# Kernel tuning notes

Hardware: AMD Instinct MI355X
Metric: run time of the kernel (lower is better)

Reference implementation:

```python
import jax, jax.numpy as jnp
from jax import lax
import numpy as np

B, DIM, H, W = 1, 48, 192, 192
HEADS, K, DIL = 2, 7, 3
HD = DIM // HEADS
HID = int(DIM * 2.66)  # 127 (Restormer GEGLU hidden)
EPS = 1e-5


def _window_starts(L, Kk, D):
    # NATTEN window-start rule: keep phase i % D, shift window inside bounds.
    s = np.zeros(L, dtype=np.int32)
    for i in range(L):
        if D <= 1:
            st = max(i - Kk // 2, 0)
            if i + Kk // 2 >= L:
                st = L - Kk
        else:
            st = i - (Kk // 2) * D
            if st < 0:
                st = i % D
            elif i + (Kk // 2) * D >= L:
                imodd = i % D
                a = (L // D) * D
                b = L - a
                if imodd < b:
                    st = L - b + imodd - 2 * (Kk // 2) * D
                else:
                    st = a + imodd - Kk * D
        s[i] = st
    return s


def _nbr_tables(L, Kk, D):
    st = _window_starts(L, Kk, D)
    idx = st[:, None] + np.arange(Kk)[None, :] * D          # [L, K] absolute neighbor idx
    pb = (st - np.arange(L)) // D                            # signed offset of window start (in dilation units)
    pb = pb[:, None] + (Kk - 1) + np.arange(Kk)[None, :]     # [L, K] rpb index in [0, 2K-2]
    return jnp.asarray(idx), jnp.asarray(pb)

IH, PBH = _nbr_tables(H, K, DIL)
IW, PBW = _nbr_tables(W, K, DIL)


def layernorm(x, w, b):  # channel LN on NCHW (WithBias, biased var)
    mu = x.mean(1, keepdims=True)
    var = ((x - mu) ** 2).mean(1, keepdims=True)
    return (x - mu) / jnp.sqrt(var + EPS) * w[None, :, None, None] + b[None, :, None, None]


def na2d(x, qkv_w, qkv_b, rpb, proj_w, proj_b):
    # x: NCHW -> BHWC
    t = x.transpose(0, 2, 3, 1)
    qkv = t @ qkv_w.T + qkv_b                                # [B,H,W,3*DIM]
    qkv = qkv.reshape(B, H, W, 3, HEADS, HD)
    q, k, v = qkv[:, :, :, 0], qkv[:, :, :, 1], qkv[:, :, :, 2]
    q = q * (HD ** -0.5)
    # gather dilated 7x7 neighborhoods: [B, H, K, W, K, heads, hd]
    kn = k[:, IH[:, :, None, None], IW[None, None, :, :]]
    vn = v[:, IH[:, :, None, None], IW[None, None, :, :]]
    attn = jnp.einsum('bijnc,bixjync->bijnxy', q, kn)        # [B,H,W,heads,K,K]
    bias = rpb[:, PBH][:, :, :, PBW]                         # [heads,H,K,W,K]
    attn = attn + bias.transpose(1, 3, 0, 2, 4)
    attn = jax.nn.softmax(attn.reshape(B, H, W, HEADS, K * K), axis=-1)
    attn = attn.reshape(B, H, W, HEADS, K, K)
    out = jnp.einsum('bijnxy,bixjync->bijnc', attn, vn).reshape(B, H, W, DIM)
    out = out @ proj_w.T + proj_b
    return out.transpose(0, 3, 1, 2)


def chan_mod(x, eca_w):  # ECA-style gate: GAP -> 1D conv over channels -> sigmoid
    p = x.mean((2, 3))                                       # [B,C]
    y = lax.conv_general_dilated(p[:, None, :], eca_w[None, None, :], (1,), [(3, 3)],
                                 dimension_numbers=('NCH', 'OIH', 'NCH'))[:, 0, :]
    return jax.nn.sigmoid(y)[:, :, None, None]


def ffn(x, w_in, w_dw, w_out):  # conv-GEGLU
    t = jnp.einsum('bchw,oc->bohw', x, w_in)                 # 1x1: DIM -> 2*HID
    t = lax.conv_general_dilated(t, w_dw, (1, 1), [(1, 1), (1, 1)],
                                 feature_group_count=2 * HID,
                                 dimension_numbers=('NCHW', 'OIHW', 'NCHW'))
    x1, x2 = t[:, :HID], t[:, HID:]
    g = jax.nn.gelu(x1, approximate=False) * x2
    return jnp.einsum('bchw,oc->bohw', g, w_out)             # 1x1: HID -> DIM


def setup_inputs() -> dict:
    key = jax.random.key(0)
    ks = jax.random.split(key, 10)
    d = {
        'x': jax.random.normal(ks[0], (B, DIM, H, W), jnp.float32),
        'ln1_w': jnp.ones((DIM,), jnp.float32),
        'ln1_b': jnp.zeros((DIM,), jnp.float32),
        'qkv_w': jax.random.normal(ks[1], (3 * DIM, DIM), jnp.float32) * 0.05,
        'qkv_b': jnp.zeros((3 * DIM,), jnp.float32),
        'rpb': jax.random.normal(ks[2], (HEADS, 2 * K - 1, 2 * K - 1), jnp.float32) * 0.02,
        'proj_w': jax.random.normal(ks[3], (DIM, DIM), jnp.float32) * 0.05,
        'proj_b': jnp.zeros((DIM,), jnp.float32),
        'eca_w': jax.random.normal(ks[4], (7,), jnp.float32) * 0.1,
        'ln2_w': jnp.ones((DIM,), jnp.float32),
        'ln2_b': jnp.zeros((DIM,), jnp.float32),
        'w_in': jax.random.normal(ks[5], (2 * HID, DIM), jnp.float32) * 0.05,
        'w_dw': jax.random.normal(ks[6], (2 * HID, 1, 3, 3), jnp.float32) * 0.05,
        'w_out': jax.random.normal(ks[7], (DIM, HID), jnp.float32) * 0.05,
    }
    return d


def reference(x, ln1_w, ln1_b, qkv_w, qkv_b, rpb, proj_w, proj_b, eca_w,
              ln2_w, ln2_b, w_in, w_dw, w_out):
    xn1 = layernorm(x, ln1_w, ln1_b)
    x = x + na2d(xn1, qkv_w, qkv_b, rpb, proj_w, proj_b) * chan_mod(xn1, eca_w)
    x = x + ffn(layernorm(x, ln2_w, ln2_b), w_in, w_dw, w_out)
    return x
```

## Files before the change

### kernel.cpp

```cpp
#include <hip/hip_runtime.h>
#include <hip/hip_bf16.h>
#include <math.h>

#define HW_ (192*192)
#define Wd 192
#define HIDc 127
#define NBLK1 (HW_/64)

#define O_LN1W 0
#define O_QKVW 96
#define O_QKVB 7008
#define O_RPB  7152
#define O_PROJW 7490
#define O_PROJB 9794
#define O_ECA  9842
#define O_LN2W 9849
#define O_WIN  9945
#define O_WDW  22137
#define O_WOUT 24423
#define WTS_LEN 30519

typedef unsigned short ushort_t;

__device__ __forceinline__ float b2f(__hip_bfloat16 v){ return __bfloat162float(v); }
__device__ __forceinline__ float u2f(ushort_t h){ return __uint_as_float(((unsigned)h)<<16); }
__device__ __forceinline__ ushort_t f2u(float f){
    __hip_bfloat16 h = __float2bfloat16(f);
    union { __hip_bfloat16 b; ushort_t u; } c; c.b = h; return c.u;
}
__device__ __forceinline__ void up2(unsigned u, float& a, float& b){
    a = __uint_as_float(u << 16);
    b = __uint_as_float(u & 0xffff0000u);
}

__device__ __forceinline__ int wstart(int i){
    if (i < 9) return i % 3;
    if (i >= 183) return 171 + (i % 3);
    return i - 9;
}

__device__ __forceinline__ float dot48bf(const uint4* wr, const float* xr){
    float acc = 0.f;
    #pragma unroll
    for (int c8 = 0; c8 < 6; c8++){
        uint4 u = wr[c8];
        float f0,f1,f2,f3,f4,f5,f6,f7;
        up2(u.x,f0,f1); up2(u.y,f2,f3); up2(u.z,f4,f5); up2(u.w,f6,f7);
        acc += f0*xr[8*c8]   + f1*xr[8*c8+1] + f2*xr[8*c8+2] + f3*xr[8*c8+3]
             + f4*xr[8*c8+4] + f5*xr[8*c8+5] + f6*xr[8*c8+6] + f7*xr[8*c8+7];
    }
    return acc;
}

__global__ void convert_kernel(
    const void* p0, const void* p1, const void* p2, const void* p3,
    const void* p4, const void* p5, const void* p6, const void* p7,
    const void* p8, const void* p9, const void* p10, const void* p11,
    const void* p12, const ushort_t* __restrict__ xu, int* __restrict__ mode_out,
    float* __restrict__ wts, ushort_t* __restrict__ qkvbf, ushort_t* __restrict__ woutTbf,
    ushort_t* __restrict__ winbf, ushort_t* __restrict__ projbf)
{
    __shared__ int sbad;
    if (threadIdx.x == 0) sbad = 0;
    __syncthreads();
    {
        unsigned u = xu[2*threadIdx.x];
        float f = __uint_as_float(u << 16);
        if (!(fabsf(f) < 100.f)) atomicAdd(&sbad, 1);
    }
    __syncthreads();
    const int md = (sbad > 16) ? 1 : 0;
    if (blockIdx.x == 0 && threadIdx.x == 0) mode_out[0] = md;

    const void* ps[13] = {p0,p1,p2,p3,p4,p5,p6,p7,p8,p9,p10,p11,p12};
    const int sz[13]  = {48,48,6912,144,338,2304,48,7,48,48,12192,2286,6096};
    const int off[13] = {O_LN1W,48,O_QKVW,O_QKVB,O_RPB,O_PROJW,O_PROJB,O_ECA,
                         O_LN2W,9897,O_WIN,O_WDW,O_WOUT};
    int b = blockIdx.x;
    if (b >= 13){
        if (b == 13){
            if (md){
                const float* s = (const float*)p2;
                for (int i = threadIdx.x; i < 6912; i += 256) qkvbf[i] = f2u(s[i]);
            } else {
                const ushort_t* s = (const ushort_t*)p2;
                for (int i = threadIdx.x; i < 6912; i += 256) qkvbf[i] = s[i];
            }
        } else if (b == 14){
            if (md){
                const float* s = (const float*)p12;
                for (int i = threadIdx.x; i < 6096; i += 256){
                    int c = i / 48, o = i - c*48;
                    woutTbf[i] = f2u(s[o*127 + c]);
                }
            } else {
                const ushort_t* s = (const ushort_t*)p12;
                for (int i = threadIdx.x; i < 6096; i += 256){
                    int c = i / 48, o = i - c*48;
                    woutTbf[i] = s[o*127 + c];
                }
            }
        } else if (b == 15){
            if (md){
                const float* s = (const float*)p10;
                for (int i = threadIdx.x; i < 12192; i += 256) winbf[i] = f2u(s[i]);
            } else {
                const ushort_t* s = (const ushort_t*)p10;
                for (int i = threadIdx.x; i < 12192; i += 256) winbf[i] = s[i];
            }
        } else {
            if (md){
                const float* s = (const float*)p5;
                for (int i = threadIdx.x; i < 2304; i += 256) projbf[i] = f2u(s[i]);
            } else {
                const ushort_t* s = (const ushort_t*)p5;
                for (int i = threadIdx.x; i < 2304; i += 256) projbf[i] = s[i];
            }
        }
        return;
    }
    int n = sz[b];
    float* dst = wts + off[b];
    if (md){
        const float* s = (const float*)ps[b];
        for (int i = threadIdx.x; i < n; i += 256) dst[i] = s[i];
    } else {
        const __hip_bfloat16* s = (const __hip_bfloat16*)ps[b];
        for (int i = threadIdx.x; i < n; i += 256) dst[i] = b2f(s[i]);
    }
}

__global__ __launch_bounds__(384) void ln1qkv_kernel(
    const void* __restrict__ x, const int* __restrict__ mode,
    const float* __restrict__ wts, const ushort_t* __restrict__ qkvbf,
    ushort_t* __restrict__ q, ushort_t* __restrict__ k, ushort_t* __restrict__ v,
    float* __restrict__ chpart)
{
    __shared__ float sx[64*49];

    const int tid  = threadIdx.x;
    const int px_l = tid & 63;
    const int r6   = __builtin_amdgcn_readfirstlane(tid >> 6);
    const int p0   = blockIdx.x * 64;
    const int p    = p0 + px_l;

    if (mode[0]){
        const float* xf = (const float*)x;
        for (int idx = tid; idx < 64*48; idx += 384){
            int c = idx >> 6, pl = idx & 63;
            sx[pl*49 + c] = xf[c*HW_ + p0 + pl];
        }
    } else {
        const __hip_bfloat16* xb = (const __hip_bfloat16*)x;
        for (int idx = tid; idx < 64*48; idx += 384){
            int c = idx >> 6, pl = idx & 63;
            sx[pl*49 + c] = b2f(xb[c*HW_ + p0 + pl]);
        }
    }
    __syncthreads();

    float xr[48];
    float mu = 0.f;
    #pragma unroll
    for (int c = 0; c < 48; c++){ xr[c] = sx[px_l*49 + c]; mu += xr[c]; }
    mu *= (1.f/48.f);
    float var = 0.f;
    #pragma unroll
    for (int c = 0; c < 48; c++){ float d = xr[c]-mu; var += d*d; }
    var *= (1.f/48.f);
    float rs = rsqrtf(var + 1e-5f);
    #pragma unroll
    for (int c = 0; c < 48; c++)
        xr[c] = (xr[c]-mu)*rs*wts[O_LN1W + c] + wts[O_LN1W + 48 + c];

    if (tid < 64){
        #pragma unroll
        for (int c = 0; c < 48; c++){
            float s = xr[c];
            s += __shfl_xor(s, 1);  s += __shfl_xor(s, 2);  s += __shfl_xor(s, 4);
            s += __shfl_xor(s, 8);  s += __shfl_xor(s, 16); s += __shfl_xor(s, 32);
            if (tid == 0) chpart[blockIdx.x*48 + c] = s;
        }
    }

    const int rbase = r6 * 24;
    const float scale = (r6 < 2) ? 0.20412414523193154f : 1.0f;
    float ov[24];
    #pragma unroll 4
    for (int ro = 0; ro < 24; ro++){
        int r = rbase + ro;
        float acc = wts[O_QKVB + r]
                  + dot48bf((const uint4*)(qkvbf + r*48), xr);
        ov[ro] = acc * scale;
    }

    unsigned int pk[12];
    #pragma unroll
    for (int d = 0; d < 12; d++)
        pk[d] = (unsigned)f2u(ov[2*d]) | ((unsigned)f2u(ov[2*d+1]) << 16);
    ushort_t* tp = (r6 >> 1) == 0 ? q : ((r6 >> 1) == 1 ? k : v);
    uint4* dst4 = (uint4*)(tp + (size_t)p*48 + (r6 & 1)*24);
    dst4[0] = make_uint4(pk[0], pk[1], pk[2],  pk[3]);
    dst4[1] = make_uint4(pk[4], pk[5], pk[6],  pk[7]);
    dst4[2] = make_uint4(pk[8], pk[9], pk[10], pk[11]);
}

__global__ __launch_bounds__(256) void gatered_kernel(
    const float* __restrict__ chpart, float* __restrict__ msum)
{
    __shared__ float red[4];
    const int c = blockIdx.x;
    const int tid = threadIdx.x;
    float acc = 0.f;
    for (int b = tid; b < NBLK1; b += 256)
        acc += chpart[b*48 + c];
    acc += __shfl_xor(acc, 1);  acc += __shfl_xor(acc, 2);  acc += __shfl_xor(acc, 4);
    acc += __shfl_xor(acc, 8);  acc += __shfl_xor(acc, 16); acc += __shfl_xor(acc, 32);
    if ((tid & 63) == 0) red[tid >> 6] = acc;
    __syncthreads();
    if (tid == 0)
        msum[c] = (red[0] + red[1] + red[2] + red[3]) * (1.f / (float)HW_);
}

__global__ void gate_kernel(const float* __restrict__ msum,
                            const float* __restrict__ wts,
                            float* __restrict__ gate)
{
    __shared__ float m[48];
    int t = threadIdx.x;
    if (t < 48) m[t] = msum[t];
    __syncthreads();
    if (t < 48){
        float a = 0.f;
        for (int kk = 0; kk < 7; kk++){
            int cc = t + kk - 3;
            if (cc >= 0 && cc < 48) a += wts[O_ECA + kk] * m[cc];
        }
        gate[t] = 1.f / (1.f + expf(-a));
    }
}

__global__ __launch_bounds__(256) void attn_kernel(
    const ushort_t* __restrict__ q, const ushort_t* __restrict__ k,
    const ushort_t* __restrict__ v, const float* __restrict__ wts,
    ushort_t* __restrict__ aout)
{
    const int head = blockIdx.y;
    __shared__ float srpb[169];
    for (int i = threadIdx.x; i < 169; i += 256) srpb[i] = wts[O_RPB + head*169 + i];
    __syncthreads();

    const int tid    = threadIdx.x;
    const int half   = tid & 1;
    const int parity = (tid >> 1) & 1;
    const int px     = blockIdx.x * 64 + (tid >> 2);
    const int i = px / Wd, j = px % Wd;
    const int sti = wstart(i), stj = wstart(j);
    const int pbi = (sti - i) / 3 + 6;
    const int pbj = (stj - j) / 3 + 6;
    const int choff = head*24 + half*12;

    float qr[12];
    {
        const ushort4* qp = (const ushort4*)(q + (size_t)px*48 + choff);
        #pragma unroll
        for (int b = 0; b < 3; b++){
            ushort4 uu = qp[b];
            qr[4*b]   = u2f(uu.x); qr[4*b+1] = u2f(uu.y);
            qr[4*b+2] = u2f(uu.z); qr[4*b+3] = u2f(uu.w);
        }
    }

    float m = -1e30f, s = 0.f;
    float acc[12];
    #pragma unroll
    for (int c = 0; c < 12; c++) acc[c] = 0.f;

    #pragma unroll
    for (int t = 0; t < 25; t++){
        int n = 2*t + parity;
        const bool inval = (n > 48);
        if (inval) n = 48;
        int xx = (n * 147) >> 10;
        int yy = n - 7*xx;
        int ii = sti + 3*xx, jj = stj + 3*yy;
        const size_t nb = (size_t)(ii*Wd + jj)*48 + choff;
        const ushort4* kp = (const ushort4*)(k + nb);
        const ushort4* vp = (const ushort4*)(v + nb);
        ushort4 k0 = kp[0], k1 = kp[1], k2 = kp[2];
        ushort4 v0 = vp[0], v1 = vp[1], v2 = vp[2];
        float d = qr[0]*u2f(k0.x) + qr[1]*u2f(k0.y)
                + qr[2]*u2f(k0.z) + qr[3]*u2f(k0.w)
                + qr[4]*u2f(k1.x) + qr[5]*u2f(k1.y)
                + qr[6]*u2f(k1.z) + qr[7]*u2f(k1.w)
                + qr[8]*u2f(k2.x) + qr[9]*u2f(k2.y)
                + qr[10]*u2f(k2.z) + qr[11]*u2f(k2.w);
        d += __shfl_xor(d, 1);
        float sc = d + srpb[(pbi+xx)*13 + (pbj+yy)];
        if (inval) sc = -1e30f;
        float mn = fmaxf(m, sc);
        float corr = __expf(m - mn);
        float p = __expf(sc - mn);
        s = s*corr + p;
        m = mn;
        acc[0]  = acc[0] *corr + p*u2f(v0.x);
        acc[1]  = acc[1] *corr + p*u2f(v0.y);
        acc[2]  = acc[2] *corr + p*u2f(v0.z);
        acc[3]  = acc[3] *corr + p*u2f(v0.w);
        acc[4]  = acc[4] *corr + p*u2f(v1.x);
        acc[5]  = acc[5] *corr + p*u2f(v1.y);
        acc[6]  = acc[6] *corr + p*u2f(v1.z);
        acc[7]  = acc[7] *corr + p*u2f(v1.w);
        acc[8]  = acc[8] *corr + p*u2f(v2.x);
        acc[9]  = acc[9] *corr + p*u2f(v2.y);
        acc[10] = acc[10]*corr + p*u2f(v2.z);
        acc[11] = acc[11]*corr + p*u2f(v2.w);
    }

    {
        float mo = __shfl_xor(m, 2);
        float so = __shfl_xor(s, 2);
        float mn = fmaxf(m, mo);
        float ca = __expf(m - mn), cb = __expf(mo - mn);
        s = s*ca + so*cb;
        #pragma unroll
        for (int c = 0; c < 12; c++)
            acc[c] = acc[c]*ca + __shfl_xor(acc[c], 2)*cb;
    }
    const float inv = 1.f / s;
    if (parity == 0){
        #pragma unroll
        for (int c = 0; c < 12; c++)
            aout[(size_t)(choff + c)*HW_ + px] = f2u(acc[c] * inv);
    }
}

__global__ __launch_bounds__(256) void proj_kernel(
    const ushort_t* __restrict__ aout, const float* __restrict__ wts,
    const ushort_t* __restrict__ projbf, const float* __restrict__ gate,
    const void* __restrict__ x, const int* __restrict__ mode,
    float* __restrict__ x2)
{
    const int tid  = threadIdx.x;
    const int px_l = tid & 63;
    const int og   = __builtin_amdgcn_readfirstlane(tid >> 6);
    const int px   = blockIdx.x * 64 + px_l;

    float ar[48];
    #pragma unroll
    for (int c = 0; c < 48; c++) ar[c] = u2f(aout[(size_t)c*HW_ + px]);

    const float* xf = (const float*)x;
    const __hip_bfloat16* xb = (const __hip_bfloat16*)x;
    const int md = mode[0];
    const int ob = og * 12;
    #pragma unroll 2
    for (int oo = 0; oo < 12; oo++){
        int o = ob + oo;
        float acc = wts[O_PROJB + o]
                  + dot48bf((const uint4*)(projbf + o*48), ar);
        float res = md ? xf[o*HW_ + px] : b2f(xb[o*HW_ + px]);
        x2[o*HW_ + px] = res + acc * gate[o];
    }
}

__global__ __launch_bounds__(256) void pw1_kernel(
    const float* __restrict__ x2, const float* __restrict__ wts,
    const ushort_t* __restrict__ winbf, ushort_t* __restrict__ t)
{
    const int tid  = threadIdx.x;
    const int px_l = tid & 63;
    const int og   = __builtin_amdgcn_readfirstlane(tid >> 6);
    const int px   = blockIdx.x * 64 + px_l;

    float xr[48];
    float mu = 0.f;
    #pragma unroll
    for (int c = 0; c < 48; c++){ xr[c] = x2[c*HW_ + px]; mu += xr[c]; }
    mu *= (1.f/48.f);
    float var = 0.f;
    #pragma unroll
    for (int c = 0; c < 48; c++){ float d = xr[c]-mu; var += d*d; }
    var *= (1.f/48.f);
    float rs = rsqrtf(var + 1e-5f);
    #pragma unroll
    for (int c = 0; c < 48; c++)
        xr[c] = (xr[c]-mu)*rs*wts[O_LN2W + c] + wts[O_LN2W + 48 + c];

    const int base = blockIdx.y * 128 + og * 32;
    for (int t2 = 0; t2 < 32; t2 += 2){
        int o0 = base + t2;
        if (o0 >= 254) break;
        const uint4* wA = (const uint4*)(winbf + o0*48);
        const uint4* wB = (const uint4*)(winbf + min(o0+1,253)*48);
        float accA = 0.f, accB = 0.f;
        #pragma unroll
        for (int c8 = 0; c8 < 6; c8++){
            uint4 ua = wA[c8];
            uint4 ub = wB[c8];
            float a0,a1,a2,a3,a4,a5,a6,a7, b0,b1,b2,b3,b4,b5,b6,b7;
            up2(ua.x,a0,a1); up2(ua.y,a2,a3); up2(ua.z,a4,a5); up2(ua.w,a6,a7);
            up2(ub.x,b0,b1); up2(ub.y,b2,b3); up2(ub.z,b4,b5); up2(ub.w,b6,b7);
            accA += a0*xr[8*c8]   + a1*xr[8*c8+1] + a2*xr[8*c8+2] + a3*xr[8*c8+3]
                  + a4*xr[8*c8+4] + a5*xr[8*c8+5] + a6*xr[8*c8+6] + a7*xr[8*c8+7];
            accB += b0*xr[8*c8]   + b1*xr[8*c8+1] + b2*xr[8*c8+2] + b3*xr[8*c8+3]
                  + b4*xr[8*c8+4] + b5*xr[8*c8+5] + b6*xr[8*c8+6] + b7*xr[8*c8+7];
        }
        t[(size_t)o0*HW_ + px] = f2u(accA);
        if (o0+1 < 254) t[(size_t)(o0+1)*HW_ + px] = f2u(accB);
    }
}

__global__ __launch_bounds__(256) void dw_kernel(
    const ushort_t* __restrict__ t, const float* __restrict__ wts,
    ushort_t* __restrict__ g)
{
    const int ch = blockIdx.y;
    const int pp = (blockIdx.x * 256 + threadIdx.x) * 2;
    const int i  = pp / Wd, j = pp % Wd;
    float w1[9], w2[9];
    #pragma unroll
    for (int s = 0; s < 9; s++){
        w1[s] = wts[O_WDW + ch*9 + s];
        w2[s] = wts[O_WDW + (ch+HIDc)*9 + s];
    }
    const ushort_t* t1 = t + (size_t)ch * HW_;
    const ushort_t* t2 = t + (size_t)(ch+HIDc) * HW_;
    float a1x = 0.f, a1y = 0.f, a2x = 0.f, a2y = 0.f;
    #pragma unroll
    for (int di = 0; di < 3; di++){
        int ii = i + di - 1;
        if (ii < 0 || ii >= 192) continue;
        int base = ii*Wd + j;
        float r0 = (j   > 0)   ? u2f(t1[base-1]) : 0.f;
        float r1 = u2f(t1[base]);
        float r2 = u2f(t1[base+1]);
        float r3 = (j+2 < 192) ? u2f(t1[base+2]) : 0.f;
        float s0 = (j   > 0)   ? u2f(t2[base-1]) : 0.f;
        float s1 = u2f(t2[base]);
        float s2 = u2f(t2[base+1]);
        float s3 = (j+2 < 192) ? u2f(t2[base+2]) : 0.f;
        float wa = w1[di*3], wb = w1[di*3+1], wc = w1[di*3+2];
        a1x += wa*r0 + wb*r1 + wc*r2;
        a1y += wa*r1 + wb*r2 + wc*r3;
        wa = w2[di*3]; wb = w2[di*3+1]; wc = w2[di*3+2];
        a2x += wa*s0 + wb*s1 + wc*s2;
        a2y += wa*s1 + wb*s2 + wc*s3;
    }
    float gx = a1x * 0.5f * (1.f + erff(a1x * 0.70710678118654752f)) * a2x;
    float gy = a1y * 0.5f * (1.f + erff(a1y * 0.70710678118654752f)) * a2y;
    unsigned pk = (unsigned)f2u(gx) | ((unsigned)f2u(gy) << 16);
    *(unsigned*)(g + (size_t)ch*HW_ + pp) = pk;
}

__global__ __launch_bounds__(128) void pw2_kernel(
    const ushort_t* __restrict__ g, const ushort_t* __restrict__ woutTbf,
    const float* __restrict__ x2, void* __restrict__ outv,
    const int* __restrict__ mode)
{
    const int ob = blockIdx.y * 12;
    const int p  = blockIdx.x * 128 + threadIdx.x;
    float acc[12];
    #pragma unroll
    for (int o = 0; o < 12; o++) acc[o] = 0.f;
    #pragma unroll 4
    for (int c = 0; c < 127; c++){
        float gv = u2f(g[(size_t)c*HW_ + p]);
        const unsigned* wr = (const unsigned*)(woutTbf + c*48 + ob);
        #pragma unroll
        for (int d = 0; d < 6; d++){
            float w0, w1;
            up2(wr[d], w0, w1);
            acc[2*d]   += w0*gv;
            acc[2*d+1] += w1*gv;
        }
    }
    if (mode[0]){
        float* out = (float*)outv;
        #pragma unroll
        for (int o = 0; o < 12; o++){
            int oc = ob + o;
            out[(size_t)oc*HW_ + p] = x2[(size_t)oc*HW_ + p] + acc[o];
        }
    } else {
        __hip_bfloat16* out = (__hip_bfloat16*)outv;
        #pragma unroll
        for (int o = 0; o < 12; o++){
            int oc = ob + o;
            out[(size_t)oc*HW_ + p] =
                __float2bfloat16(x2[(size_t)oc*HW_ + p] + acc[o]);
        }
    }
}

extern "C" void kernel_launch(void* const* d_in, const int* in_sizes, int n_in,
                              void* d_out, int out_size, void* d_ws, size_t ws_size,
                              hipStream_t stream)
{
    (void)in_sizes; (void)n_in; (void)out_size;

    char* ws = (char*)d_ws;
    ushort_t* q    = (ushort_t*)(ws);
    ushort_t* k    = (ushort_t*)(ws + 3538944);
    ushort_t* v    = (ushort_t*)(ws + 7077888);
    ushort_t* aout = (ushort_t*)(ws + 10616832);
    ushort_t* t    = (ushort_t*)(ws);
    float*    x2   = (float*)   (ws + 18726912);
    ushort_t* g    = (ushort_t*)(ws + 25804800);
    float*    gate = (float*)   (ws + 35168448);
    int*      mode = (int*)     (ws + 35168640);
    float*    wts  = (float*)   (ws + 35168656);
    float*    chpart=(float*)   (ws + 35168656 + (size_t)WTS_LEN*4);
    float*    msum = chpart + (size_t)NBLK1*48;
    ushort_t* qkvbf= (ushort_t*)(msum + 48);
    ushort_t* woutTbf = qkvbf + 6912;
    ushort_t* winbf   = woutTbf + 6096;
    ushort_t* projbf  = winbf + 12192;

    size_t need = 35168656 + (size_t)WTS_LEN*4 + (size_t)NBLK1*48*4 + 48*4
                + (6912 + 6096 + 12192 + 2304)*2;
    if (ws_size < need) return;

    convert_kernel<<<17, 256, 0, stream>>>(
        d_in[1], d_in[2], d_in[3], d_in[4], d_in[5], d_in[6], d_in[7],
        d_in[8], d_in[9], d_in[10], d_in[11], d_in[12], d_in[13],
        (const ushort_t*)d_in[0], mode, wts, qkvbf, woutTbf, winbf, projbf);

    ln1qkv_kernel<<<dim3(NBLK1), 384, 0, stream>>>(d_in[0], mode, wts, qkvbf,
                                                   q, k, v, chpart);
    gatered_kernel<<<48, 256, 0, stream>>>(chpart, msum);
    gate_kernel<<<1, 64, 0, stream>>>(msum, wts, gate);
    attn_kernel<<<dim3(HW_/64, 2), 256, 0, stream>>>(q, k, v, wts, aout);
    proj_kernel<<<dim3(HW_/64), 256, 0, stream>>>(aout, wts, projbf, gate,
                                                  d_in[0], mode, x2);
    pw1_kernel<<<dim3(HW_/64, 2), 256, 0, stream>>>(x2, wts, winbf, t);
    dw_kernel<<<dim3(HW_/512, 127), 256, 0, stream>>>(t, wts, g);
    pw2_kernel<<<dim3(HW_/128, 4), 128, 0, stream>>>(g, woutTbf, x2, d_out, mode);
}
```

Measured before the change: 248.1 us.

## Pad QKV per-head groups to 32-byte slots and store residual in bf16

The q/k/v buffers are re-laid out so each pixel occupies 64 bf16 slots, with each 12-channel half-head group in an aligned 16-element slot. The attention kernel can then fetch each group with one uint4 and one uint2 load instead of three ushort4 loads. Separately, the intermediate residual x2 is stored as bf16 instead of fp32, halving its traffic in the proj, pw1 and pw2 kernels. The costs are a larger q/k/v footprint (padding bytes fetched per neighbor) and a loss of precision in the residual stream.

Result: slower. 258.6 us (+4.2%).

```diff
diff --git a/kernel.cpp b/kernel.cpp
--- a/kernel.cpp
+++ b/kernel.cpp
@@ -199,10 +199,13 @@
     for (int d = 0; d < 12; d++)
         pk[d] = (unsigned)f2u(ov[2*d]) | ((unsigned)f2u(ov[2*d+1]) << 16);
     ushort_t* tp = (r6 >> 1) == 0 ? q : ((r6 >> 1) == 1 ? k : v);
-    uint4* dst4 = (uint4*)(tp + (size_t)p*48 + (r6 & 1)*24);
-    dst4[0] = make_uint4(pk[0], pk[1], pk[2],  pk[3]);
-    dst4[1] = make_uint4(pk[4], pk[5], pk[6],  pk[7]);
-    dst4[2] = make_uint4(pk[8], pk[9], pk[10], pk[11]);
+    const int h = r6 & 1;
+    ushort_t* b0 = tp + (size_t)p*64 + h*32;
+    *(uint4*)b0        = make_uint4(pk[0], pk[1], pk[2], pk[3]);
+    *(uint2*)(b0 + 8)  = make_uint2(pk[4], pk[5]);
+    ushort_t* b1 = b0 + 16;
+    *(uint4*)b1        = make_uint4(pk[6], pk[7], pk[8], pk[9]);
+    *(uint2*)(b1 + 8)  = make_uint2(pk[10], pk[11]);
 }
 
 __global__ __launch_bounds__(256) void gatered_kernel(
@@ -258,17 +261,17 @@
     const int sti = wstart(i), stj = wstart(j);
     const int pbi = (sti - i) / 3 + 6;
     const int pbj = (stj - j) / 3 + 6;
+    const int grp   = head*2 + half;
     const int choff = head*24 + half*12;
 
     float qr[12];
     {
-        const ushort4* qp = (const ushort4*)(q + (size_t)px*48 + choff);
-        #pragma unroll
-        for (int b = 0; b < 3; b++){
-            ushort4 uu = qp[b];
-            qr[4*b]   = u2f(uu.x); qr[4*b+1] = u2f(uu.y);
-            qr[4*b+2] = u2f(uu.z); qr[4*b+3] = u2f(uu.w);
-        }
+        const ushort_t* qb = q + (size_t)px*64 + grp*16;
+        uint4 qa = *(const uint4*)qb;
+        uint2 qc = *(const uint2*)(qb + 8);
+        up2(qa.x, qr[0], qr[1]); up2(qa.y, qr[2], qr[3]);
+        up2(qa.z, qr[4], qr[5]); up2(qa.w, qr[6], qr[7]);
+        up2(qc.x, qr[8], qr[9]); up2(qc.y, qr[10], qr[11]);
     }
 
     float m = -1e30f, s = 0.f;
@@ -284,17 +287,19 @@
         int xx = (n * 147) >> 10;
         int yy = n - 7*xx;
         int ii = sti + 3*xx, jj = stj + 3*yy;
-        const size_t nb = (size_t)(ii*Wd + jj)*48 + choff;
-        const ushort4* kp = (const ushort4*)(k + nb);
-        const ushort4* vp = (const ushort4*)(v + nb);
-        ushort4 k0 = kp[0], k1 = kp[1], k2 = kp[2];
-        ushort4 v0 = vp[0], v1 = vp[1], v2 = vp[2];
-        float d = qr[0]*u2f(k0.x) + qr[1]*u2f(k0.y)
-                + qr[2]*u2f(k0.z) + qr[3]*u2f(k0.w)
-                + qr[4]*u2f(k1.x) + qr[5]*u2f(k1.y)
-                + qr[6]*u2f(k1.z) + qr[7]*u2f(k1.w)
-                + qr[8]*u2f(k2.x) + qr[9]*u2f(k2.y)
-                + qr[10]*u2f(k2.z) + qr[11]*u2f(k2.w);
+        const size_t nb = (size_t)(ii*Wd + jj)*64 + grp*16;
+        const ushort_t* kb = k + nb;
+        const ushort_t* vb = v + nb;
+        uint4 ka = *(const uint4*)kb;
+        uint2 kc = *(const uint2*)(kb + 8);
+        uint4 va = *(const uint4*)vb;
+        uint2 vc = *(const uint2*)(vb + 8);
+        float k0,k1,k2,k3,k4,k5,k6,k7,k8,k9,k10,k11;
+        up2(ka.x,k0,k1); up2(ka.y,k2,k3); up2(ka.z,k4,k5); up2(ka.w,k6,k7);
+        up2(kc.x,k8,k9); up2(kc.y,k10,k11);
+        float d = qr[0]*k0 + qr[1]*k1 + qr[2]*k2 + qr[3]*k3
+                + qr[4]*k4 + qr[5]*k5 + qr[6]*k6 + qr[7]*k7
+                + qr[8]*k8 + qr[9]*k9 + qr[10]*k10 + qr[11]*k11;
         d += __shfl_xor(d, 1);
         float sc = d + srpb[(pbi+xx)*13 + (pbj+yy)];
         if (inval) sc = -1e30f;
@@ -303,18 +308,21 @@
         float p = __expf(sc - mn);
         s = s*corr + p;
         m = mn;
-        acc[0]  = acc[0] *corr + p*u2f(v0.x);
-        acc[1]  = acc[1] *corr + p*u2f(v0.y);
-        acc[2]  = acc[2] *corr + p*u2f(v0.z);
-        acc[3]  = acc[3] *corr + p*u2f(v0.w);
-        acc[4]  = acc[4] *corr + p*u2f(v1.x);
-        acc[5]  = acc[5] *corr + p*u2f(v1.y);
-        acc[6]  = acc[6] *corr + p*u2f(v1.z);
-        acc[7]  = acc[7] *corr + p*u2f(v1.w);
-        acc[8]  = acc[8] *corr + p*u2f(v2.x);
-        acc[9]  = acc[9] *corr + p*u2f(v2.y);
-        acc[10] = acc[10]*corr + p*u2f(v2.z);
-        acc[11] = acc[11]*corr + p*u2f(v2.w);
+        float v0,v1,v2,v3,v4,v5,v6,v7,v8,v9,v10,v11;
+        up2(va.x,v0,v1); up2(va.y,v2,v3); up2(va.z,v4,v5); up2(va.w,v6,v7);
+        up2(vc.x,v8,v9); up2(vc.y,v10,v11);
+        acc[0]  = acc[0] *corr + p*v0;
+        acc[1]  = acc[1] *corr + p*v1;
+        acc[2]  = acc[2] *corr + p*v2;
+        acc[3]  = acc[3] *corr + p*v3;
+        acc[4]  = acc[4] *corr + p*v4;
+        acc[5]  = acc[5] *corr + p*v5;
+        acc[6]  = acc[6] *corr + p*v6;
+        acc[7]  = acc[7] *corr + p*v7;
+        acc[8]  = acc[8] *corr + p*v8;
+        acc[9]  = acc[9] *corr + p*v9;
+        acc[10] = acc[10]*corr + p*v10;
+        acc[11] = acc[11]*corr + p*v11;
     }
 
     {
@@ -339,7 +347,7 @@
     const ushort_t* __restrict__ aout, const float* __restrict__ wts,
     const ushort_t* __restrict__ projbf, const float* __restrict__ gate,
     const void* __restrict__ x, const int* __restrict__ mode,
-    float* __restrict__ x2)
+    ushort_t* __restrict__ x2)
 {
     const int tid  = threadIdx.x;
     const int px_l = tid & 63;
@@ -360,12 +368,12 @@
         float acc = wts[O_PROJB + o]
                   + dot48bf((const uint4*)(projbf + o*48), ar);
         float res = md ? xf[o*HW_ + px] : b2f(xb[o*HW_ + px]);
-        x2[o*HW_ + px] = res + acc * gate[o];
+        x2[(size_t)o*HW_ + px] = f2u(res + acc * gate[o]);
     }
 }
 
 __global__ __launch_bounds__(256) void pw1_kernel(
-    const float* __restrict__ x2, const float* __restrict__ wts,
+    const ushort_t* __restrict__ x2, const float* __restrict__ wts,
     const ushort_t* __restrict__ winbf, ushort_t* __restrict__ t)
 {
     const int tid  = threadIdx.x;
@@ -376,7 +384,7 @@
     float xr[48];
     float mu = 0.f;
     #pragma unroll
-    for (int c = 0; c < 48; c++){ xr[c] = x2[c*HW_ + px]; mu += xr[c]; }
+    for (int c = 0; c < 48; c++){ xr[c] = u2f(x2[(size_t)c*HW_ + px]); mu += xr[c]; }
     mu *= (1.f/48.f);
     float var = 0.f;
     #pragma unroll
@@ -455,7 +463,7 @@
 
 __global__ __launch_bounds__(128) void pw2_kernel(
     const ushort_t* __restrict__ g, const ushort_t* __restrict__ woutTbf,
-    const float* __restrict__ x2, void* __restrict__ outv,
+    const ushort_t* __restrict__ x2, void* __restrict__ outv,
     const int* __restrict__ mode)
 {
     const int ob = blockIdx.y * 12;
@@ -480,7 +488,7 @@
         #pragma unroll
         for (int o = 0; o < 12; o++){
             int oc = ob + o;
-            out[(size_t)oc*HW_ + p] = x2[(size_t)oc*HW_ + p] + acc[o];
+            out[(size_t)oc*HW_ + p] = u2f(x2[(size_t)oc*HW_ + p]) + acc[o];
         }
     } else {
         __hip_bfloat16* out = (__hip_bfloat16*)outv;
@@ -488,7 +496,7 @@
         for (int o = 0; o < 12; o++){
             int oc = ob + o;
             out[(size_t)oc*HW_ + p] =
-                __float2bfloat16(x2[(size_t)oc*HW_ + p] + acc[o]);
+                __float2bfloat16(u2f(x2[(size_t)oc*HW_ + p]) + acc[o]);
         }
     }
 }
@@ -501,12 +509,12 @@
 
     char* ws = (char*)d_ws;
     ushort_t* q    = (ushort_t*)(ws);
-    ushort_t* k    = (ushort_t*)(ws + 3538944);
-    ushort_t* v    = (ushort_t*)(ws + 7077888);
-    ushort_t* aout = (ushort_t*)(ws + 10616832);
+    ushort_t* k    = (ushort_t*)(ws + 4718592);
+    ushort_t* v    = (ushort_t*)(ws + 9437184);
+    ushort_t* aout = (ushort_t*)(ws + 14155776);
     ushort_t* t    = (ushort_t*)(ws);
-    float*    x2   = (float*)   (ws + 18726912);
-    ushort_t* g    = (ushort_t*)(ws + 25804800);
+    ushort_t* x2   = (ushort_t*)(ws + 18726912);
+    ushort_t* g    = (ushort_t*)(ws + 22265856);
     float*    gate = (float*)   (ws + 35168448);
     int*      mode = (int*)     (ws + 35168640);
     float*    wts  = (float*)   (ws + 35168656);
```
